# Kernel optimization log

Hardware: AMD Instinct MI355X
Metric: run time of the kernel (lower is better)

## Reference

```python
import jax, jax.numpy as jnp
import numpy as np

N, M = 50000, 12
ORIG, NBR_F, AF = 92, 41, 64
B, NA = 500, 100
NCONV = 3
BN_EPS = 1e-5


def _batchnorm(x, g, b):
    # training-mode batchnorm over axis 0 (biased variance, like torch)
    mu = jnp.mean(x, axis=0)
    var = jnp.mean((x - mu) ** 2, axis=0)
    return (x - mu) * jax.lax.rsqrt(var + BN_EPS) * g + b


def _conv_layer(atom, nbr_fea, nbr_idx, W, bW, g1, b1, g2, b2):
    n, m = nbr_idx.shape
    atom_nbr = atom[nbr_idx]                                   # [N,M,AF] gather
    center = jnp.broadcast_to(atom[:, None, :], (n, m, AF))
    total = jnp.concatenate([center, atom_nbr, nbr_fea], axis=2)  # [N,M,2AF+NBR_F]
    gated = jnp.einsum('nmf,of->nmo', total, W) + bW              # [N,M,2AF]
    gated = _batchnorm(gated.reshape(-1, 2 * AF), g1, b1).reshape(n, m, 2 * AF)
    filt, core = gated[..., :AF], gated[..., AF:]
    summed = jnp.sum(jax.nn.sigmoid(filt) * jax.nn.softplus(core), axis=1)  # [N,AF]
    summed = _batchnorm(summed, g2, b2)
    return jax.nn.softplus(atom + summed)


def setup_inputs() -> dict:
    key = jax.random.key(0)
    ks = jax.random.split(key, 12)
    inp = {
        'atom_fea': jax.random.normal(ks[0], (N, ORIG), jnp.float32),
        'nbr_fea': jax.random.normal(ks[1], (N, M, NBR_F), jnp.float32),
        'nbr_fea_idx': jax.random.randint(ks[2], (N, M), 0, N, jnp.int32),
        'crystal_atom_idx': jnp.arange(B * NA, dtype=jnp.int32).reshape(B, NA),
        'mask': jnp.ones((ORIG,), jnp.float32),
        'emb_W': jax.random.normal(ks[3], (AF, ORIG), jnp.float32) * 0.05,
        'conv_W': jax.random.normal(ks[4], (NCONV, 2 * AF, 2 * AF + NBR_F), jnp.float32) * 0.05,
        'conv_b': jnp.zeros((NCONV, 2 * AF), jnp.float32),
        'bn1_g': jnp.ones((NCONV, 2 * AF), jnp.float32),
        'bn1_b': jnp.zeros((NCONV, 2 * AF), jnp.float32),
        'bn2_g': jnp.ones((NCONV, AF), jnp.float32),
        'bn2_b': jnp.zeros((NCONV, AF), jnp.float32),
        'fc1_W': jax.random.normal(ks[5], (AF, AF), jnp.float32) * 0.05,
        'fc1_b': jnp.zeros((AF,), jnp.float32),
        'fc2_W': jax.random.normal(ks[6], (AF, AF), jnp.float32) * 0.05,
        'fc2_b': jnp.zeros((AF,), jnp.float32),
        'out_W': jax.random.normal(ks[7], (1, AF), jnp.float32) * 0.05,
        'out_b': jnp.zeros((1,), jnp.float32),
    }
    return inp


def reference(atom_fea, nbr_fea, nbr_fea_idx, crystal_atom_idx, mask, emb_W,
              conv_W, conv_b, bn1_g, bn1_b, bn2_g, bn2_b,
              fc1_W, fc1_b, fc2_W, fc2_b, out_W, out_b):
    x = atom_fea * mask                      # learned input mask
    atom_mask_feature = x
    h = x @ emb_W.T                          # embedding, no bias -> [N,AF]
    for i in range(NCONV):
        h = _conv_layer(h, nbr_fea, nbr_fea_idx, conv_W[i], conv_b[i],
                        bn1_g[i], bn1_b[i], bn2_g[i], bn2_b[i])
    g = h[crystal_atom_idx]                  # [B,NA,AF]
    norm = jnp.sqrt(jnp.sum(g * g, axis=-1, keepdims=True))
    g = g / jnp.maximum(norm, 1e-12)         # F.normalize p=2
    pooled = jnp.mean(g, axis=1)             # [B,AF]
    z = jax.nn.softplus(pooled @ fc1_W.T + fc1_b)
    z = jax.nn.softplus(z @ fc2_W.T + fc2_b)
    props = z @ out_W.T + out_b              # [B,1]
    return props, atom_mask_feature
```

## Files before the change

kernel.cpp:

```cpp
#include <hip/hip_runtime.h>
#include <hip/hip_bf16.h>
#include <stdint.h>

#define NN      50000
#define MMN     12
#define NMROWS  600000
#define ORIGF   92
#define NBRF    41
#define AFD     64
#define GCH     128
#define KTOT    169
#define BBC     500
#define NAA     100
#define BN_EPS  1e-5f
#define GROWS   96

typedef unsigned short u16;
typedef __attribute__((ext_vector_type(8))) short bf16x8;
typedef __attribute__((ext_vector_type(4))) float f32x4;

__device__ __forceinline__ float b2f(u16 u) {
    union { uint32_t i; float f; } v; v.i = ((uint32_t)u) << 16; return v.f;
}
__device__ __forceinline__ float hi2f(uint32_t p) {
    union { uint32_t i; float f; } v; v.i = p & 0xffff0000u; return v.f;
}
__device__ __forceinline__ u16 f2b(float f) {
    __hip_bfloat16 h = __float2bfloat16(f);
    return *(u16*)&h;
}
__device__ __forceinline__ float sp_f(float x) {
    return fmaxf(x, 0.f) + __logf(1.f + __expf(-fabsf(x)));
}
__device__ __forceinline__ float sigm_f(float x) {
    return __builtin_amdgcn_rcpf(1.f + __expf(-x));
}

__global__ void k_mask(const float* __restrict__ atom, const float* __restrict__ mask,
                       float* __restrict__ dout) {
    int i = blockIdx.x * blockDim.x + threadIdx.x;
    int stride = gridDim.x * blockDim.x;
    for (; i < NN * ORIGF; i += stride) {
        int k = i % ORIGF;
        dout[BBC + i] = atom[i] * mask[k];
    }
}

__global__ __launch_bounds__(256, 2) void k_emb(const float* __restrict__ atom,
                                                const float* __restrict__ mask,
                                                const float* __restrict__ embW,
                                                u16* __restrict__ h) {
    __shared__ float xs[4 * 96];
    int lane = threadIdx.x & 63;
    int w = threadIdx.x >> 6;
    float wr[ORIGF];
#pragma unroll
    for (int k = 0; k < ORIGF; ++k) wr[k] = embW[lane * ORIGF + k];
    float m1 = mask[lane];
    float m2 = (lane < ORIGF - 64) ? mask[64 + lane] : 0.f;
    for (int base = blockIdx.x * 4; base < NN; base += gridDim.x * 4) {
        int n = base + w;
        xs[w * 96 + lane] = atom[(size_t)n * ORIGF + lane] * m1;
        if (lane < ORIGF - 64)
            xs[w * 96 + 64 + lane] = atom[(size_t)n * ORIGF + 64 + lane] * m2;
        __syncthreads();
        float acc = 0.f;
#pragma unroll
        for (int k4 = 0; k4 < ORIGF / 4; ++k4) {
            float4 f = *(const float4*)&xs[w * 96 + 4 * k4];
            acc += f.x * wr[4*k4] + f.y * wr[4*k4+1] + f.z * wr[4*k4+2] + f.w * wr[4*k4+3];
        }
        h[(size_t)n * AFD + lane] = f2b(acc);
        __syncthreads();
    }
}

__global__ __launch_bounds__(256, 2) void k_cn(const u16* __restrict__ h,
                                               const float* __restrict__ convW,
                                               uint32_t* __restrict__ C32) {
    __shared__ float xs[2 * AFD];
    int lane = threadIdx.x & 63;
    int w = threadIdx.x >> 6;
    int half = w & 1;
    int sub = w >> 1;
    int koff = half * AFD;
    float wa[AFD], wb[AFD];
#pragma unroll
    for (int k = 0; k < AFD; ++k) {
        wa[k] = convW[lane * KTOT + koff + k];
        wb[k] = convW[(lane + 64) * KTOT + koff + k];
    }
    for (int base = blockIdx.x * 2; base < NN; base += gridDim.x * 2) {
        int n = base + sub;
        if (half == 0) xs[sub * AFD + lane] = b2f(h[(size_t)n * AFD + lane]);
        __syncthreads();
        float aa = 0.f, ab = 0.f;
#pragma unroll
        for (int k4 = 0; k4 < AFD / 4; ++k4) {
            float4 f = *(const float4*)&xs[sub * AFD + 4 * k4];
            aa += f.x * wa[4*k4] + f.y * wa[4*k4+1] + f.z * wa[4*k4+2] + f.w * wa[4*k4+3];
            ab += f.x * wb[4*k4] + f.y * wb[4*k4+1] + f.z * wb[4*k4+2] + f.w * wb[4*k4+3];
        }
        C32[(size_t)n * 128 + half * 64 + lane] = (uint32_t)f2b(aa) | ((uint32_t)f2b(ab) << 16);
        __syncthreads();
    }
}

__device__ __forceinline__ void stage_nbrf(const float* nbrf, int r0, float* fs) {
    const float4* src = (const float4*)(nbrf + (size_t)r0 * NBRF);
    for (int t = threadIdx.x; t < (GROWS * NBRF) / 4; t += 256) {
        float4 f = src[t];
        float vals[4] = {f.x, f.y, f.z, f.w};
#pragma unroll
        for (int j = 0; j < 4; ++j) {
            int e = t * 4 + j;
            int row = e / NBRF;
            int k = e - row * NBRF;
            fs[row * 44 + k] = vals[j];
        }
    }
}

template<bool STORE>
__global__ __launch_bounds__(256, 4) void k_gs4(
    const uint32_t* __restrict__ C32, const float* __restrict__ nbrf,
    const int* __restrict__ nbridx, const float* __restrict__ convW,
    const float* __restrict__ convb, float* __restrict__ stats,
    uint32_t* __restrict__ gated32)
{
    __shared__ __align__(16) u16 As[GROWS * 56];
    __shared__ uint32_t C2s[GROWS * 65];
    __shared__ uint32_t C1s[8 * 65];
    const int tid  = threadIdx.x;
    const int lane = tid & 63;
    const int w    = tid >> 6;
    const int lr   = lane & 15;
    const int lg   = lane >> 4;
    const int r0    = blockIdx.x * GROWS;
    const int nbase = blockIdx.x * (GROWS / MMN);
    const int rowb  = w * 24;

    uint32_t c2v[12];
#pragma unroll
    for (int rr = 0; rr < 12; ++rr) {
        int j = nbridx[r0 + rowb + rr];
        c2v[rr] = C32[(size_t)j * 128 + 64 + lane];
    }
    uint32_t c1v[2];
#pragma unroll
    for (int q = 0; q < 2; ++q) {
        int e = tid + q * 256;
        c1v[q] = C32[(size_t)(nbase + (e >> 6)) * 128 + (e & 63)];
    }
    const float4* src4 = (const float4*)(nbrf + (size_t)r0 * NBRF);
#pragma unroll
    for (int it = 0; it < 4; ++it) {
        int t = tid + it * 256;
        if (it < 3 || t < 984) {
            float4 f = src4[t];
            float vals[4] = {f.x, f.y, f.z, f.w};
#pragma unroll
            for (int jj = 0; jj < 4; ++jj) {
                int e = t * 4 + jj;
                int row = e / NBRF;
                int k = e - row * NBRF;
                As[row * 56 + k] = f2b(vals[jj]);
            }
        }
    }
#pragma unroll
    for (int rr = 0; rr < 12; ++rr) C2s[(rowb + rr) * 65 + lane] = c2v[rr];
#pragma unroll
    for (int rr = 0; rr < 12; ++rr) {
        int j = nbridx[r0 + rowb + 12 + rr];
        c2v[rr] = C32[(size_t)j * 128 + 64 + lane];
    }
#pragma unroll
    for (int q = 0; q < 2; ++q) {
        int e = tid + q * 256;
        C1s[(e >> 6) * 65 + (e & 63)] = c1v[q];
    }
#pragma unroll
    for (int it = 0; it < 6; ++it) {
        int e = tid + it * 256;
        if (it < 5 || e < 1440) {
            int row = e / 15;
            int k = 41 + (e - row * 15);
            As[row * 56 + k] = (k == 41) ? (u16)0x3F80 : (u16)0;
        }
    }
    const int chlo = w * 16 + lr;
    const int chhi = chlo + 64;
    const float* wlo = convW + (size_t)chlo * KTOT + 128;
    const float* whi = convW + (size_t)chhi * KTOT + 128;
    bf16x8 bl0, bh0;
    bf16x8 bl1 = {0,0,0,0,0,0,0,0}, bh1 = {0,0,0,0,0,0,0,0};
#pragma unroll
    for (int e = 0; e < 8; ++e) {
        bl0[e] = (short)f2b(wlo[8 * lg + e]);
        bh0[e] = (short)f2b(whi[8 * lg + e]);
    }
    if (lg == 0) {
#pragma unroll
        for (int e = 0; e < 8; ++e) {
            bl1[e] = (short)f2b(wlo[32 + e]);
            bh1[e] = (short)f2b(whi[32 + e]);
        }
    } else if (lg == 1) {
        bl1[0] = (short)f2b(wlo[40]); bl1[1] = (short)f2b(convb[chlo]);
        bh1[0] = (short)f2b(whi[40]); bh1[1] = (short)f2b(convb[chhi]);
    }
#pragma unroll
    for (int rr = 0; rr < 12; ++rr) C2s[(rowb + 12 + rr) * 65 + lane] = c2v[rr];
    __syncthreads();

    f32x4 acc[6][2];
    const f32x4 z = {0.f, 0.f, 0.f, 0.f};
    const bf16x8 zb = {0,0,0,0,0,0,0,0};
#pragma unroll
    for (int mt = 0; mt < 6; ++mt) {
        const u16* ap = &As[(mt * 16 + lr) * 56 + 8 * lg];
        bf16x8 a0 = *(const bf16x8*)ap;
        bf16x8 a1 = zb;
        if (lg < 3) a1 = *(const bf16x8*)(ap + 32);
        acc[mt][0] = __builtin_amdgcn_mfma_f32_16x16x32_bf16(a1, bl1,
                     __builtin_amdgcn_mfma_f32_16x16x32_bf16(a0, bl0, z, 0, 0, 0), 0, 0, 0);
        acc[mt][1] = __builtin_amdgcn_mfma_f32_16x16x32_bf16(a1, bh1,
                     __builtin_amdgcn_mfma_f32_16x16x32_bf16(a0, bh0, z, 0, 0, 0), 0, 0, 0);
    }

    const int word = w * 16 + lr;
    float slo = 0.f, qlo = 0.f, shi = 0.f, qhi = 0.f;
#pragma unroll
    for (int mt = 0; mt < 6; ++mt) {
#pragma unroll
        for (int rg = 0; rg < 4; ++rg) {
            int row = mt * 16 + 4 * lg + rg;
            uint32_t p1 = C1s[(row / MMN) * 65 + word];
            uint32_t p2 = C2s[row * 65 + word];
            float glo = acc[mt][0][rg] + b2f((u16)p1) + b2f((u16)p2);
            float ghi = acc[mt][1][rg] + hi2f(p1) + hi2f(p2);
            if (STORE) {
                gated32[(size_t)(r0 + row) * 64 + word] =
                    (uint32_t)f2b(glo) | ((uint32_t)f2b(ghi) << 16);
            }
            slo += glo; qlo = fmaf(glo, glo, qlo);
            shi += ghi; qhi = fmaf(ghi, ghi, qhi);
        }
    }
    slo += __shfl_xor(slo, 16, 64); slo += __shfl_xor(slo, 32, 64);
    qlo += __shfl_xor(qlo, 16, 64); qlo += __shfl_xor(qlo, 32, 64);
    shi += __shfl_xor(shi, 16, 64); shi += __shfl_xor(shi, 32, 64);
    qhi += __shfl_xor(qhi, 16, 64); qhi += __shfl_xor(qhi, 32, 64);
    if (lane < 16) {
        atomicAdd(&stats[word], slo);
        atomicAdd(&stats[128 + word], qlo);
        atomicAdd(&stats[64 + word], shi);
        atomicAdd(&stats[128 + 64 + word], qhi);
    }
}

__global__ void k_fin(float* __restrict__ stats, const float* __restrict__ gg,
                      const float* __restrict__ bb, int nch, float invcnt,
                      int sumoff, int sqoff, int scoff, int shoff) {
    int c = threadIdx.x;
    if (c < nch) {
        float mean = stats[sumoff + c] * invcnt;
        float var  = fmaxf(stats[sqoff + c] * invcnt - mean * mean, 0.f);
        float sc   = gg[c] * rsqrtf(var + BN_EPS);
        stats[scoff + c] = sc;
        stats[shoff + c] = bb[c] - mean * sc;
    }
}

__global__ __launch_bounds__(256) void k_acts(
    const uint32_t* __restrict__ gated32, float* __restrict__ stats,
    u16* __restrict__ summed)
{
    __shared__ float red[4][64][2];
    int lane = threadIdx.x & 63;
    int w = threadIdx.x >> 6;
    float sa = stats[384 + lane],      ba = stats[512 + lane];
    float sb = stats[384 + 64 + lane], bb = stats[512 + 64 + lane];
    int wave = blockIdx.x * 4 + w, nw = gridDim.x * 4;
    float s2 = 0.f, q2 = 0.f;
    for (int n = wave; n < NN; n += nw) {
        const uint32_t* gr = gated32 + (size_t)n * MMN * 64;
        float s = 0.f;
#pragma unroll
        for (int m = 0; m < MMN; ++m) {
            uint32_t p = gr[m * 64 + lane];
            float f1 = b2f((u16)p) * sa + ba;
            float cc = hi2f(p) * sb + bb;
            s += sigm_f(f1) * sp_f(cc);
        }
        summed[(size_t)n * AFD + lane] = f2b(s);
        s2 += s; q2 += s * s;
    }
    red[w][lane][0] = s2; red[w][lane][1] = q2;
    __syncthreads();
    if (threadIdx.x < 64) {
        int c = threadIdx.x;
        float a = 0, b = 0;
#pragma unroll
        for (int ww = 0; ww < 4; ++ww) { a += red[ww][c][0]; b += red[ww][c][1]; }
        atomicAdd(&stats[256 + c], a);
        atomicAdd(&stats[320 + c], b);
    }
}

__device__ __forceinline__ void edge_dot(const float* fr, const float* wfa,
                                         const float* wfb, float& aa, float& ab) {
#pragma unroll
    for (int k4 = 0; k4 < 10; ++k4) {
        float4 f = *(const float4*)&fr[4 * k4];
        aa += f.x * wfa[4*k4] + f.y * wfa[4*k4+1] + f.z * wfa[4*k4+2] + f.w * wfa[4*k4+3];
        ab += f.x * wfb[4*k4] + f.y * wfb[4*k4+1] + f.z * wfb[4*k4+2] + f.w * wfb[4*k4+3];
    }
    aa += fr[40] * wfa[40];
    ab += fr[40] * wfb[40];
}

__global__ __launch_bounds__(256) void k_act(
    const uint32_t* __restrict__ C32, const float* __restrict__ nbrf,
    const int* __restrict__ nbridx, const float* __restrict__ convW,
    const float* __restrict__ convb, float* __restrict__ stats,
    u16* __restrict__ summed)
{
    __shared__ float fs[GROWS * 44];
    __shared__ float red[4][64][2];
    int lane = threadIdx.x & 63;
    int w = threadIdx.x >> 6;
    int r0 = blockIdx.x * GROWS;
    stage_nbrf(nbrf, r0, fs);
    float wfa[NBRF], wfb[NBRF];
#pragma unroll
    for (int k = 0; k < NBRF; ++k) {
        wfa[k] = convW[lane * KTOT + 128 + k];
        wfb[k] = convW[(lane + 64) * KTOT + 128 + k];
    }
    float biasa = convb[lane], biasb = convb[64 + lane];
    float sa = stats[384 + lane],      ba = stats[512 + lane];
    float sb = stats[384 + 64 + lane], bb = stats[512 + 64 + lane];
    __syncthreads();
    float s2 = 0.f, q2 = 0.f;
    float s = 0.f;
    float c1a = 0.f, c1b = 0.f;
    for (int rr = 0; rr < 24; ++rr) {
        int rl = w * 24 + rr;
        int r = r0 + rl;
        if ((rr % MMN) == 0) {
            int n = r / MMN;
            uint32_t p1 = C32[(size_t)n * 128 + lane];
            c1a = b2f((u16)p1); c1b = b2f((u16)(p1 >> 16));
            s = 0.f;
        }
        int j = nbridx[r];
        uint32_t p2 = C32[(size_t)j * 128 + 64 + lane];
        float aa = c1a + b2f((u16)p2) + biasa;
        float ab = c1b + b2f((u16)(p2 >> 16)) + biasb;
        edge_dot(&fs[rl * 44], wfa, wfb, aa, ab);
        float f1 = aa * sa + ba;
        float cc = ab * sb + bb;
        s += sigm_f(f1) * sp_f(cc);
        if ((rr % MMN) == MMN - 1) {
            int n = r / MMN;
            summed[(size_t)n * AFD + lane] = f2b(s);
            s2 += s; q2 += s * s;
        }
    }
    red[w][lane][0] = s2; red[w][lane][1] = q2;
    __syncthreads();
    if (threadIdx.x < 64) {
        int c = threadIdx.x;
        float a = 0, b = 0;
#pragma unroll
        for (int ww = 0; ww < 4; ++ww) { a += red[ww][c][0]; b += red[ww][c][1]; }
        atomicAdd(&stats[256 + c], a);
        atomicAdd(&stats[320 + c], b);
    }
}

__global__ void k_update(u16* __restrict__ h, const u16* __restrict__ summed,
                         const float* __restrict__ stats) {
    int i = blockIdx.x * blockDim.x + threadIdx.x;
    int st = gridDim.x * blockDim.x;
    int c = threadIdx.x & 63;
    float sc = stats[640 + c], shf = stats[704 + c];
    for (; i < NN * AFD; i += st) {
        float x = b2f(h[i]) + b2f(summed[i]) * sc + shf;
        h[i] = f2b(sp_f(x));
    }
}

__global__ __launch_bounds__(256) void k_pool(const u16* __restrict__ h,
                                              const int* __restrict__ cry,
                                              float* __restrict__ pooled) {
    __shared__ float red[4][64];
    int lane = threadIdx.x & 63, w = threadIdx.x >> 6;
    int b = blockIdx.x;
    float acc = 0.f;
    for (int a = w; a < NAA; a += 4) {
        int idx = cry[b * NAA + a];
        float v = b2f(h[(size_t)idx * AFD + lane]);
        float s2 = v * v;
#pragma unroll
        for (int o = 32; o > 0; o >>= 1) s2 += __shfl_xor(s2, o, 64);
        acc += v / fmaxf(sqrtf(s2), 1e-12f);
    }
    red[w][lane] = acc;
    __syncthreads();
    if (threadIdx.x < 64) {
        float s = red[0][threadIdx.x] + red[1][threadIdx.x] +
                  red[2][threadIdx.x] + red[3][threadIdx.x];
        pooled[b * AFD + threadIdx.x] = s * (1.f / NAA);
    }
}

__global__ __launch_bounds__(64) void k_head(const float* __restrict__ pooled,
    const float* __restrict__ fc1W, const float* __restrict__ fc1b,
    const float* __restrict__ fc2W, const float* __restrict__ fc2b,
    const float* __restrict__ outW, const float* __restrict__ outb,
    float* __restrict__ props) {
    __shared__ float W1[64 * 65], W2[64 * 65], zbuf[64], pbuf[64];
    int l = threadIdx.x;
    for (int e = l; e < 64 * 64; e += 64) {
        int o = e >> 6, k = e & 63;
        W1[o * 65 + k] = fc1W[e];
        W2[o * 65 + k] = fc2W[e];
    }
    int b = blockIdx.x;
    pbuf[l] = pooled[b * AFD + l];
    __syncthreads();
    float acc = fc1b[l];
#pragma unroll
    for (int k = 0; k < 64; ++k) acc += pbuf[k] * W1[l * 65 + k];
    zbuf[l] = sp_f(acc);
    __syncthreads();
    acc = fc2b[l];
#pragma unroll
    for (int k = 0; k < 64; ++k) acc += zbuf[k] * W2[l * 65 + k];
    float v = sp_f(acc) * outW[l];
#pragma unroll
    for (int o = 32; o > 0; o >>= 1) v += __shfl_xor(v, o, 64);
    if (l == 0) props[b] = v + outb[0];
}

extern "C" void kernel_launch(void* const* d_in, const int* in_sizes, int n_in,
                              void* d_out, int out_size, void* d_ws, size_t ws_size,
                              hipStream_t stream) {
    const float* atom  = (const float*)d_in[0];
    const float* nbrf  = (const float*)d_in[1];
    const int* nbridx  = (const int*)d_in[2];
    const int* cry     = (const int*)d_in[3];
    const float* mask  = (const float*)d_in[4];
    const float* embW  = (const float*)d_in[5];
    const float* convW = (const float*)d_in[6];
    const float* convb = (const float*)d_in[7];
    const float* bn1g  = (const float*)d_in[8];
    const float* bn1b  = (const float*)d_in[9];
    const float* bn2g  = (const float*)d_in[10];
    const float* bn2b  = (const float*)d_in[11];
    const float* fc1W  = (const float*)d_in[12];
    const float* fc1b  = (const float*)d_in[13];
    const float* fc2W  = (const float*)d_in[14];
    const float* fc2b  = (const float*)d_in[15];
    const float* outW  = (const float*)d_in[16];
    const float* outb  = (const float*)d_in[17];

    char* ws = (char*)d_ws;
    float* stats    = (float*)ws;
    float* pooled   = (float*)(ws + 4096);
    u16*   h        = (u16*)(ws + (1u << 20));
    u16*   summed   = (u16*)(ws + (8u << 20));
    uint32_t* C32   = (uint32_t*)(ws + (16u << 20));
    uint32_t* gated32 = (uint32_t*)(ws + (48u << 20));
    const bool bigws = ws_size >= (size_t)(48u << 20) + 153600000u;

    float* out_props = (float*)d_out;

    k_mask<<<2048, 256, 0, stream>>>(atom, mask, (float*)d_out);
    k_emb<<<512, 256, 0, stream>>>(atom, mask, embW, h);
    for (int i = 0; i < 3; ++i) {
        hipMemsetAsync(stats, 0, 384 * sizeof(float), stream);
        k_cn<<<1024, 256, 0, stream>>>(h, convW + (size_t)i * GCH * KTOT, C32);
        if (bigws)
            k_gs4<true><<<NMROWS / GROWS, 256, 0, stream>>>(C32, nbrf, nbridx,
                convW + (size_t)i * GCH * KTOT, convb + (size_t)i * GCH, stats, gated32);
        else
            k_gs4<false><<<NMROWS / GROWS, 256, 0, stream>>>(C32, nbrf, nbridx,
                convW + (size_t)i * GCH * KTOT, convb + (size_t)i * GCH, stats, gated32);
        k_fin<<<1, 128, 0, stream>>>(stats, bn1g + (size_t)i * GCH, bn1b + (size_t)i * GCH,
                                     128, 1.f / NMROWS, 0, 128, 384, 512);
        if (bigws)
            k_acts<<<1024, 256, 0, stream>>>(gated32, stats, summed);
        else
            k_act<<<NMROWS / GROWS, 256, 0, stream>>>(C32, nbrf, nbridx,
                convW + (size_t)i * GCH * KTOT, convb + (size_t)i * GCH, stats, summed);
        k_fin<<<1, 128, 0, stream>>>(stats, bn2g + (size_t)i * AFD, bn2b + (size_t)i * AFD,
                                     64, 1.f / NN, 256, 320, 640, 704);
        k_update<<<1024, 256, 0, stream>>>(h, summed, stats);
    }
    k_pool<<<BBC, 256, 0, stream>>>(h, cry, pooled);
    k_head<<<BBC, 64, 0, stream>>>(pooled, fc1W, fc1b, fc2W, fc2b, outW, outb, out_props);
}
```

Baseline: 1.040 ms.

## Fuse mask into embedding, MFMA node projection, fold BN finalize into consumers

The separate mask-output kernel is merged into the embedding kernel, so the atom features are read once. The per-node center/neighbor projection now runs on bf16 MFMA over 96-row tiles instead of scalar FMAs with per-row block barriers. The two one-block BN finalize kernels are removed and each consumer recomputes scale and shift from the raw sums. k_acts gets a larger grid. Together these cut launch count and global traffic, at the cost of redundant per-thread BN math and bf16 rounding of the weights.

```diff
diff --git a/kernel.cpp b/kernel.cpp
--- a/kernel.cpp
+++ b/kernel.cpp
@@ -36,20 +36,11 @@
     return __builtin_amdgcn_rcpf(1.f + __expf(-x));
 }
 
-__global__ void k_mask(const float* __restrict__ atom, const float* __restrict__ mask,
-                       float* __restrict__ dout) {
-    int i = blockIdx.x * blockDim.x + threadIdx.x;
-    int stride = gridDim.x * blockDim.x;
-    for (; i < NN * ORIGF; i += stride) {
-        int k = i % ORIGF;
-        dout[BBC + i] = atom[i] * mask[k];
-    }
-}
-
-__global__ __launch_bounds__(256, 2) void k_emb(const float* __restrict__ atom,
-                                                const float* __restrict__ mask,
-                                                const float* __restrict__ embW,
-                                                u16* __restrict__ h) {
+__global__ __launch_bounds__(256, 2) void k_embm(const float* __restrict__ atom,
+                                                 const float* __restrict__ mask,
+                                                 const float* __restrict__ embW,
+                                                 u16* __restrict__ h,
+                                                 float* __restrict__ dout) {
     __shared__ float xs[4 * 96];
     int lane = threadIdx.x & 63;
     int w = threadIdx.x >> 6;
@@ -60,9 +51,14 @@
     float m2 = (lane < ORIGF - 64) ? mask[64 + lane] : 0.f;
     for (int base = blockIdx.x * 4; base < NN; base += gridDim.x * 4) {
         int n = base + w;
-        xs[w * 96 + lane] = atom[(size_t)n * ORIGF + lane] * m1;
-        if (lane < ORIGF - 64)
-            xs[w * 96 + 64 + lane] = atom[(size_t)n * ORIGF + 64 + lane] * m2;
+        float v1 = atom[(size_t)n * ORIGF + lane] * m1;
+        xs[w * 96 + lane] = v1;
+        dout[BBC + (size_t)n * ORIGF + lane] = v1;
+        if (lane < ORIGF - 64) {
+            float v2 = atom[(size_t)n * ORIGF + 64 + lane] * m2;
+            xs[w * 96 + 64 + lane] = v2;
+            dout[BBC + (size_t)n * ORIGF + 64 + lane] = v2;
+        }
         __syncthreads();
         float acc = 0.f;
 #pragma unroll
@@ -75,34 +71,68 @@
     }
 }
 
-__global__ __launch_bounds__(256, 2) void k_cn(const u16* __restrict__ h,
-                                               const float* __restrict__ convW,
-                                               uint32_t* __restrict__ C32) {
-    __shared__ float xs[2 * AFD];
-    int lane = threadIdx.x & 63;
-    int w = threadIdx.x >> 6;
-    int half = w & 1;
-    int sub = w >> 1;
-    int koff = half * AFD;
-    float wa[AFD], wb[AFD];
-#pragma unroll
-    for (int k = 0; k < AFD; ++k) {
-        wa[k] = convW[lane * KTOT + koff + k];
-        wb[k] = convW[(lane + 64) * KTOT + koff + k];
-    }
-    for (int base = blockIdx.x * 2; base < NN; base += gridDim.x * 2) {
-        int n = base + sub;
-        if (half == 0) xs[sub * AFD + lane] = b2f(h[(size_t)n * AFD + lane]);
-        __syncthreads();
-        float aa = 0.f, ab = 0.f;
-#pragma unroll
-        for (int k4 = 0; k4 < AFD / 4; ++k4) {
-            float4 f = *(const float4*)&xs[sub * AFD + 4 * k4];
-            aa += f.x * wa[4*k4] + f.y * wa[4*k4+1] + f.z * wa[4*k4+2] + f.w * wa[4*k4+3];
-            ab += f.x * wb[4*k4] + f.y * wb[4*k4+1] + f.z * wb[4*k4+2] + f.w * wb[4*k4+3];
-        }
-        C32[(size_t)n * 128 + half * 64 + lane] = (uint32_t)f2b(aa) | ((uint32_t)f2b(ab) << 16);
-        __syncthreads();
+__global__ __launch_bounds__(256, 2) void k_cnm(const u16* __restrict__ h,
+                                                const float* __restrict__ convW,
+                                                uint32_t* __restrict__ C32) {
+    __shared__ __align__(16) u16 Hs[96 * 72];
+    const int tid  = threadIdx.x;
+    const int lane = tid & 63;
+    const int w    = tid >> 6;
+    const int lr   = lane & 15;
+    const int lg   = lane >> 4;
+    const int r0   = blockIdx.x * 96;
+    const int rows = (NN - r0 < 96) ? (NN - r0) : 96;
+
+#pragma unroll
+    for (int it = 0; it < 12; ++it) {
+        int idx = tid + it * 256;
+        int row = idx >> 5, col = idx & 31;
+        if (row < rows)
+            *(uint32_t*)&Hs[row * 72 + col * 2] =
+                ((const uint32_t*)h)[(size_t)(r0 + row) * 32 + col];
+    }
+    const int chlo = w * 16 + lr;
+    bf16x8 bfr[4][2];
+#pragma unroll
+    for (int v = 0; v < 4; ++v) {
+        int ch = chlo + (v & 1) * 64;
+        int q  = v >> 1;
+        const float* bp = convW + (size_t)ch * KTOT + q * 64;
+#pragma unroll
+        for (int e = 0; e < 8; ++e) {
+            bfr[v][0][e] = (short)f2b(bp[8 * lg + e]);
+            bfr[v][1][e] = (short)f2b(bp[32 + 8 * lg + e]);
+        }
+    }
+    __syncthreads();
+
+    f32x4 acc[6][4];
+    const f32x4 z = {0.f, 0.f, 0.f, 0.f};
+#pragma unroll
+    for (int mt = 0; mt < 6; ++mt) {
+        if (mt * 16 < rows) {
+            const u16* ap = &Hs[(mt * 16 + lr) * 72 + 8 * lg];
+            bf16x8 a0 = *(const bf16x8*)ap;
+            bf16x8 a1 = *(const bf16x8*)(ap + 32);
+#pragma unroll
+            for (int v = 0; v < 4; ++v)
+                acc[mt][v] = __builtin_amdgcn_mfma_f32_16x16x32_bf16(a1, bfr[v][1],
+                             __builtin_amdgcn_mfma_f32_16x16x32_bf16(a0, bfr[v][0], z, 0, 0, 0), 0, 0, 0);
+        }
+    }
+#pragma unroll
+    for (int mt = 0; mt < 6; ++mt) {
+#pragma unroll
+        for (int rg = 0; rg < 4; ++rg) {
+            int row = mt * 16 + 4 * lg + rg;
+            if (row < rows) {
+                size_t n = r0 + row;
+                C32[n * 128 + chlo] =
+                    (uint32_t)f2b(acc[mt][0][rg]) | ((uint32_t)f2b(acc[mt][1][rg]) << 16);
+                C32[n * 128 + 64 + chlo] =
+                    (uint32_t)f2b(acc[mt][2][rg]) | ((uint32_t)f2b(acc[mt][3][rg]) << 16);
+            }
+        }
     }
 }
 
@@ -260,28 +290,23 @@
     }
 }
 
-__global__ void k_fin(float* __restrict__ stats, const float* __restrict__ gg,
-                      const float* __restrict__ bb, int nch, float invcnt,
-                      int sumoff, int sqoff, int scoff, int shoff) {
-    int c = threadIdx.x;
-    if (c < nch) {
-        float mean = stats[sumoff + c] * invcnt;
-        float var  = fmaxf(stats[sqoff + c] * invcnt - mean * mean, 0.f);
-        float sc   = gg[c] * rsqrtf(var + BN_EPS);
-        stats[scoff + c] = sc;
-        stats[shoff + c] = bb[c] - mean * sc;
-    }
-}
-
 __global__ __launch_bounds__(256) void k_acts(
-    const uint32_t* __restrict__ gated32, float* __restrict__ stats,
-    u16* __restrict__ summed)
+    const uint32_t* __restrict__ gated32, const float* __restrict__ stats,
+    const float* __restrict__ g1, const float* __restrict__ b1,
+    float* __restrict__ ostats, u16* __restrict__ summed)
 {
     __shared__ float red[4][64][2];
     int lane = threadIdx.x & 63;
     int w = threadIdx.x >> 6;
-    float sa = stats[384 + lane],      ba = stats[512 + lane];
-    float sb = stats[384 + 64 + lane], bb = stats[512 + 64 + lane];
+    const float invn = 1.f / (float)NMROWS;
+    float m1 = stats[lane] * invn;
+    float v1 = fmaxf(stats[128 + lane] * invn - m1 * m1, 0.f);
+    float sa = g1[lane] * rsqrtf(v1 + BN_EPS);
+    float ba = b1[lane] - m1 * sa;
+    float m2 = stats[64 + lane] * invn;
+    float v2 = fmaxf(stats[192 + lane] * invn - m2 * m2, 0.f);
+    float sb = g1[64 + lane] * rsqrtf(v2 + BN_EPS);
+    float bb = b1[64 + lane] - m2 * sb;
     int wave = blockIdx.x * 4 + w, nw = gridDim.x * 4;
     float s2 = 0.f, q2 = 0.f;
     for (int n = wave; n < NN; n += nw) {
@@ -304,8 +329,8 @@
         float a = 0, b = 0;
 #pragma unroll
         for (int ww = 0; ww < 4; ++ww) { a += red[ww][c][0]; b += red[ww][c][1]; }
-        atomicAdd(&stats[256 + c], a);
-        atomicAdd(&stats[320 + c], b);
+        atomicAdd(&ostats[256 + c], a);
+        atomicAdd(&ostats[320 + c], b);
     }
 }
 
@@ -324,7 +349,8 @@
 __global__ __launch_bounds__(256) void k_act(
     const uint32_t* __restrict__ C32, const float* __restrict__ nbrf,
     const int* __restrict__ nbridx, const float* __restrict__ convW,
-    const float* __restrict__ convb, float* __restrict__ stats,
+    const float* __restrict__ convb, const float* __restrict__ g1,
+    const float* __restrict__ b1, float* __restrict__ stats,
     u16* __restrict__ summed)
 {
     __shared__ float fs[GROWS * 44];
@@ -340,8 +366,15 @@
         wfb[k] = convW[(lane + 64) * KTOT + 128 + k];
     }
     float biasa = convb[lane], biasb = convb[64 + lane];
-    float sa = stats[384 + lane],      ba = stats[512 + lane];
-    float sb = stats[384 + 64 + lane], bb = stats[512 + 64 + lane];
+    const float invn = 1.f / (float)NMROWS;
+    float m1 = stats[lane] * invn;
+    float v1 = fmaxf(stats[128 + lane] * invn - m1 * m1, 0.f);
+    float sa = g1[lane] * rsqrtf(v1 + BN_EPS);
+    float ba = b1[lane] - m1 * sa;
+    float m2 = stats[64 + lane] * invn;
+    float v2 = fmaxf(stats[192 + lane] * invn - m2 * m2, 0.f);
+    float sb = g1[64 + lane] * rsqrtf(v2 + BN_EPS);
+    float bb = b1[64 + lane] - m2 * sb;
     __syncthreads();
     float s2 = 0.f, q2 = 0.f;
     float s = 0.f;
@@ -382,11 +415,16 @@
 }
 
 __global__ void k_update(u16* __restrict__ h, const u16* __restrict__ summed,
-                         const float* __restrict__ stats) {
+                         const float* __restrict__ stats,
+                         const float* __restrict__ g2, const float* __restrict__ b2) {
     int i = blockIdx.x * blockDim.x + threadIdx.x;
     int st = gridDim.x * blockDim.x;
     int c = threadIdx.x & 63;
-    float sc = stats[640 + c], shf = stats[704 + c];
+    const float invn = 1.f / (float)NN;
+    float m = stats[256 + c] * invn;
+    float var = fmaxf(stats[320 + c] * invn - m * m, 0.f);
+    float sc = g2[c] * rsqrtf(var + BN_EPS);
+    float shf = b2[c] - m * sc;
     for (; i < NN * AFD; i += st) {
         float x = b2f(h[i]) + b2f(summed[i]) * sc + shf;
         h[i] = f2b(sp_f(x));
@@ -479,27 +517,24 @@
 
     float* out_props = (float*)d_out;
 
-    k_mask<<<2048, 256, 0, stream>>>(atom, mask, (float*)d_out);
-    k_emb<<<512, 256, 0, stream>>>(atom, mask, embW, h);
+    k_embm<<<512, 256, 0, stream>>>(atom, mask, embW, h, (float*)d_out);
     for (int i = 0; i < 3; ++i) {
         hipMemsetAsync(stats, 0, 384 * sizeof(float), stream);
-        k_cn<<<1024, 256, 0, stream>>>(h, convW + (size_t)i * GCH * KTOT, C32);
-        if (bigws)
+        k_cnm<<<(NN + 95) / 96, 256, 0, stream>>>(h, convW + (size_t)i * GCH * KTOT, C32);
+        if (bigws) {
             k_gs4<true><<<NMROWS / GROWS, 256, 0, stream>>>(C32, nbrf, nbridx,
                 convW + (size_t)i * GCH * KTOT, convb + (size_t)i * GCH, stats, gated32);
-        else
+            k_acts<<<2048, 256, 0, stream>>>(gated32, stats,
+                bn1g + (size_t)i * GCH, bn1b + (size_t)i * GCH, stats, summed);
+        } else {
             k_gs4<false><<<NMROWS / GROWS, 256, 0, stream>>>(C32, nbrf, nbridx,
                 convW + (size_t)i * GCH * KTOT, convb + (size_t)i * GCH, stats, gated32);
-        k_fin<<<1, 128, 0, stream>>>(stats, bn1g + (size_t)i * GCH, bn1b + (size_t)i * GCH,
-                                     128, 1.f / NMROWS, 0, 128, 384, 512);
-        if (bigws)
-            k_acts<<<1024, 256, 0, stream>>>(gated32, stats, summed);
-        else
             k_act<<<NMROWS / GROWS, 256, 0, stream>>>(C32, nbrf, nbridx,
-                convW + (size_t)i * GCH * KTOT, convb + (size_t)i * GCH, stats, summed);
-        k_fin<<<1, 128, 0, stream>>>(stats, bn2g + (size_t)i * AFD, bn2b + (size_t)i * AFD,
-                                     64, 1.f / NN, 256, 320, 640, 704);
-        k_update<<<1024, 256, 0, stream>>>(h, summed, stats);
+                convW + (size_t)i * GCH * KTOT, convb + (size_t)i * GCH,
+                bn1g + (size_t)i * GCH, bn1b + (size_t)i * GCH, stats, summed);
+        }
+        k_update<<<1024, 256, 0, stream>>>(h, summed, stats,
+            bn2g + (size_t)i * AFD, bn2b + (size_t)i * AFD);
     }
     k_pool<<<BBC, 256, 0, stream>>>(h, cry, pooled);
     k_head<<<BBC, 64, 0, stream>>>(pooled, fc1W, fc1b, fc2W, fc2b, outW, outb, out_props);
```

New measurement: 963.1 us. 1.08x faster.
